# Kernel tuning notes

Measured on AMD Instinct MI355X. Metric: run time of the kernel, lower is better.

## Reference

```python
import jax, jax.numpy as jnp
import numpy as np

B, S, E, H, D = 4, 2048, 1024, 8, 256  # batch, seq, embed_dim, heads, hidden_units


def setup_inputs() -> dict:
    key = jax.random.key(0)
    ks = jax.random.split(key, 9)
    scale = 0.02
    return {
        "inputA": jax.random.normal(ks[0], (B, S, E), dtype=jnp.float32),
        "WQ": jax.random.normal(ks[1], (H, E, D), dtype=jnp.float32) * scale,
        "bQ": jnp.zeros((H, D), dtype=jnp.float32),
        "WK": jax.random.normal(ks[2], (H, E, D), dtype=jnp.float32) * scale,
        "bK": jnp.zeros((H, D), dtype=jnp.float32),
        "WV": jax.random.normal(ks[3], (H, E, D), dtype=jnp.float32) * scale,
        "bV": jnp.zeros((H, D), dtype=jnp.float32),
        "WZ": jax.random.normal(ks[4], (H * D, E), dtype=jnp.float32) * scale,
        "bZ": jnp.zeros((E,), dtype=jnp.float32),
    }


def reference(inputA, WQ, bQ, WK, bK, WV, bV, WZ, bZ):
    # Per-head Linear -> ReLU (dropout=0 -> identity); heads stacked on axis h.
    Q = jax.nn.relu(jnp.einsum('bse,hed->bhsd', inputA, WQ) + bQ[None, :, None, :])
    K = jax.nn.relu(jnp.einsum('bse,hed->bhsd', inputA, WK) + bK[None, :, None, :])
    V = jax.nn.relu(jnp.einsum('bse,hed->bhsd', inputA, WV) + bV[None, :, None, :])
    # scores[b,h,s,t] ; torch bmm output was [B, S, T] per head
    scores = jnp.einsum('bhsd,bhtd->bhst', Q, K) / jnp.sqrt(jnp.float32(E))
    # double softmax: torch dim=1 (query axis s) then dim=2 (key axis t)
    A = jax.nn.softmax(scores, axis=2)
    A = jax.nn.softmax(A, axis=3)
    Z = jnp.einsum('bhst,bhtd->bhsd', A, V)
    # concat heads along feature dim (head order matches torch cat)
    Zall = Z.transpose(0, 2, 1, 3).reshape(B, S, H * D)
    return Zall @ WZ + bZ
```

## Files before the change

### kernel.cpp

```cpp
#include <hip/hip_runtime.h>

typedef __attribute__((ext_vector_type(8))) short short8;
typedef __attribute__((ext_vector_type(4))) float f32x4;

constexpr int B_ = 4, S_ = 2048, E_ = 1024, H_ = 8, D_ = 256;
constexpr int HD_ = H_ * D_;
constexpr int BS_ = B_ * S_;
constexpr int BH_ = B_ * H_;
constexpr float INV_SQRT_E = 0.03125f;

__device__ __forceinline__ unsigned short f2bf(float f) {
    union { float f; unsigned u; } x; x.f = f;
    unsigned r = (x.u + 0x7fffu + ((x.u >> 16) & 1u)) >> 16;
    return (unsigned short)r;
}

__device__ __forceinline__ void gl_lds16(const void* g, void* lds) {
    __builtin_amdgcn_global_load_lds((const __attribute__((address_space(1))) void*)g,
                                     (__attribute__((address_space(3))) void*)lds, 16, 0, 0);
}

__global__ __launch_bounds__(256) void cast_k(const float* __restrict__ src,
                                              unsigned short* __restrict__ dst, int n4) {
    int i = blockIdx.x * 256 + threadIdx.x;
    if (i >= n4) return;
    float4 v = reinterpret_cast<const float4*>(src)[i];
    ushort4 o;
    o.x = f2bf(v.x); o.y = f2bf(v.y); o.z = f2bf(v.z); o.w = f2bf(v.w);
    reinterpret_cast<ushort4*>(dst)[i] = o;
}

__global__ __launch_bounds__(256) void tcast_k(const float* __restrict__ src,
                                               unsigned short* __restrict__ dst, int R, int C) {
    __shared__ float tile[32][33];
    int b = blockIdx.z;
    const float* s = src + (size_t)b * R * C;
    unsigned short* d = dst + (size_t)b * R * C;
    int c0 = blockIdx.x * 32, r0 = blockIdx.y * 32;
    int tx = threadIdx.x, ty = threadIdx.y;
#pragma unroll
    for (int i = 0; i < 4; ++i)
        tile[ty + i * 8][tx] = s[(size_t)(r0 + ty + i * 8) * C + c0 + tx];
    __syncthreads();
#pragma unroll
    for (int i = 0; i < 4; ++i)
        d[(size_t)(c0 + ty + i * 8) * R + r0 + tx] = f2bf(tile[tx][ty + i * 8]);
}

__global__ __launch_bounds__(256) void tbf_k(const unsigned short* __restrict__ src,
                                             unsigned short* __restrict__ dst) {
    __shared__ unsigned short tile[32][33];
    int bh = blockIdx.z;
    int d0 = blockIdx.x * 32, s0 = blockIdx.y * 32;
    int tx = threadIdx.x, ty = threadIdx.y;
#pragma unroll
    for (int i = 0; i < 4; ++i)
        tile[ty + i * 8][tx] = src[((size_t)bh * S_ + s0 + ty + i * 8) * D_ + d0 + tx];
    __syncthreads();
#pragma unroll
    for (int i = 0; i < 4; ++i)
        dst[((size_t)bh * D_ + d0 + ty + i * 8) * S_ + s0 + tx] = tile[tx][ty + i * 8];
}

__global__ __launch_bounds__(256) void gemm_qkv_k(const unsigned short* __restrict__ A,
                                                  const unsigned short* __restrict__ Bt,
                                                  const float* __restrict__ bias,
                                                  unsigned short* __restrict__ out) {
    __shared__ __align__(16) unsigned short As[128 * 32];
    __shared__ __align__(16) unsigned short Bs[128 * 32];
    const int tid = threadIdx.x;
    const int wave = tid >> 6, lane = tid & 63;
    const int quad = lane >> 4, l15 = lane & 15;
    const int wm = wave >> 1, wn = wave & 1;
    const int m0 = blockIdx.y * 128, n0 = blockIdx.x * 128;
    const int c1 = tid, c2 = tid + 256;
    const int r1 = c1 >> 2, kc1 = (c1 & 3) * 8;
    const int r2 = c2 >> 2, kc2 = (c2 & 3) * 8;
    char* aB1 = (char*)As + wave * 1024; char* aB2 = aB1 + 4096;
    char* bB1 = (char*)Bs + wave * 1024; char* bB2 = bB1 + 4096;
    const unsigned short* a1 = A + (size_t)(m0 + r1) * E_ + kc1;
    const unsigned short* a2 = A + (size_t)(m0 + r2) * E_ + kc2;
    const unsigned short* b1 = Bt + (size_t)(n0 + r1) * E_ + kc1;
    const unsigned short* b2 = Bt + (size_t)(n0 + r2) * E_ + kc2;
    f32x4 acc[4][4] = {};
    for (int k0 = 0; k0 < E_; k0 += 32) {
        __syncthreads();
        gl_lds16(a1 + k0, aB1);
        gl_lds16(a2 + k0, aB2);
        gl_lds16(b1 + k0, bB1);
        gl_lds16(b2 + k0, bB2);
        __syncthreads();
        short8 af[4], bf[4];
        const short* Ass = (const short*)As;
        const short* Bss = (const short*)Bs;
#pragma unroll
        for (int f = 0; f < 4; ++f) {
            af[f] = *(const short8*)&Ass[(wm * 64 + f * 16 + l15) * 32 + quad * 8];
            bf[f] = *(const short8*)&Bss[(wn * 64 + f * 16 + l15) * 32 + quad * 8];
        }
#pragma unroll
        for (int fm = 0; fm < 4; ++fm)
#pragma unroll
            for (int fn = 0; fn < 4; ++fn)
                acc[fm][fn] = __builtin_amdgcn_mfma_f32_16x16x32_bf16(af[fm], bf[fn], acc[fm][fn], 0, 0, 0);
    }
#pragma unroll
    for (int fm = 0; fm < 4; ++fm) {
        int mbase = m0 + wm * 64 + fm * 16 + quad * 4;
#pragma unroll
        for (int fn = 0; fn < 4; ++fn) {
            int n = n0 + wn * 64 + fn * 16 + l15;
            int h = n >> 8, d = n & 255;
            float bv = bias[n];
#pragma unroll
            for (int r = 0; r < 4; ++r) {
                int m = mbase + r;
                int b = m >> 11, s = m & 2047;
                float v = fmaxf(acc[fm][fn][r] + bv, 0.0f);
                out[((size_t)(b * H_ + h) * S_ + s) * D_ + d] = f2bf(v);
            }
        }
    }
}

__global__ __launch_bounds__(256) void gemm_out_k(const unsigned short* __restrict__ A,
                                                  const unsigned short* __restrict__ Bt,
                                                  const float* __restrict__ bias,
                                                  float* __restrict__ out) {
    __shared__ __align__(16) unsigned short As[128 * 32];
    __shared__ __align__(16) unsigned short Bs[128 * 32];
    const int tid = threadIdx.x;
    const int wave = tid >> 6, lane = tid & 63;
    const int quad = lane >> 4, l15 = lane & 15;
    const int wm = wave >> 1, wn = wave & 1;
    const int m0 = blockIdx.y * 128, n0 = blockIdx.x * 128;
    const int c1 = tid, c2 = tid + 256;
    const int r1 = c1 >> 2, kc1 = (c1 & 3) * 8;
    const int r2 = c2 >> 2, kc2 = (c2 & 3) * 8;
    char* aB1 = (char*)As + wave * 1024; char* aB2 = aB1 + 4096;
    char* bB1 = (char*)Bs + wave * 1024; char* bB2 = bB1 + 4096;
    const unsigned short* a1 = A + (size_t)(m0 + r1) * HD_ + kc1;
    const unsigned short* a2 = A + (size_t)(m0 + r2) * HD_ + kc2;
    const unsigned short* b1 = Bt + (size_t)(n0 + r1) * HD_ + kc1;
    const unsigned short* b2 = Bt + (size_t)(n0 + r2) * HD_ + kc2;
    f32x4 acc[4][4] = {};
    for (int k0 = 0; k0 < HD_; k0 += 32) {
        __syncthreads();
        gl_lds16(a1 + k0, aB1);
        gl_lds16(a2 + k0, aB2);
        gl_lds16(b1 + k0, bB1);
        gl_lds16(b2 + k0, bB2);
        __syncthreads();
        short8 af[4], bf[4];
        const short* Ass = (const short*)As;
        const short* Bss = (const short*)Bs;
#pragma unroll
        for (int f = 0; f < 4; ++f) {
            af[f] = *(const short8*)&Ass[(wm * 64 + f * 16 + l15) * 32 + quad * 8];
            bf[f] = *(const short8*)&Bss[(wn * 64 + f * 16 + l15) * 32 + quad * 8];
        }
#pragma unroll
        for (int fm = 0; fm < 4; ++fm)
#pragma unroll
            for (int fn = 0; fn < 4; ++fn)
                acc[fm][fn] = __builtin_amdgcn_mfma_f32_16x16x32_bf16(af[fm], bf[fn], acc[fm][fn], 0, 0, 0);
    }
#pragma unroll
    for (int fm = 0; fm < 4; ++fm) {
        int mbase = m0 + wm * 64 + fm * 16 + quad * 4;
#pragma unroll
        for (int fn = 0; fn < 4; ++fn) {
            int n = n0 + wn * 64 + fn * 16 + l15;
            float bv = bias[n];
#pragma unroll
            for (int r = 0; r < 4; ++r)
                out[(size_t)(mbase + r) * E_ + n] = acc[fm][fn][r] + bv;
        }
    }
}

__global__ __launch_bounds__(512, 2) void colsum_k(const unsigned short* __restrict__ Q,
                                                   const unsigned short* __restrict__ K,
                                                   float* __restrict__ invLcol) {
    __shared__ float part[8][64];
    const int tid = threadIdx.x;
    const int wave = tid >> 6, lane = tid & 63;
    const int quad = lane >> 4, l15 = lane & 15;
    const int tg = wave >> 2, sg = wave & 3;
    const int p = blockIdx.x;
    const int bh = (p & 7) + 8 * ((p >> 3) >> 4);
    const int t0 = ((p >> 3) & 15) * 128;
    const unsigned short* Qh = Q + (size_t)bh * S_ * D_;
    const unsigned short* Kh = K + (size_t)bh * S_ * D_;
    short8 kf[32];
#pragma unroll
    for (int kc = 0; kc < 8; ++kc)
#pragma unroll
        for (int fm = 0; fm < 4; ++fm)
            kf[kc * 4 + fm] = *(const short8*)&Kh[(size_t)(t0 + tg * 64 + fm * 16 + l15) * D_ + kc * 32 + quad * 8];
    float rl[4][4] = {};
    const unsigned short* Qw = Qh + (size_t)(sg * 16 + l15) * D_ + quad * 8;
    short8 qf[8];
#pragma unroll
    for (int kc = 0; kc < 8; ++kc) qf[kc] = *(const short8*)&Qw[kc * 32];
    for (int s0 = 0; s0 < S_; s0 += 64) {
        f32x4 acc[4] = {};
#pragma unroll
        for (int kc = 0; kc < 8; ++kc)
#pragma unroll
            for (int fm = 0; fm < 4; ++fm)
                acc[fm] = __builtin_amdgcn_mfma_f32_16x16x32_bf16(kf[kc * 4 + fm], qf[kc], acc[fm], 0, 0, 0);
        int sn = (s0 + 64) & (S_ - 1);
#pragma unroll
        for (int kc = 0; kc < 8; ++kc)
            qf[kc] = *(const short8*)&Qw[(size_t)sn * D_ + kc * 32];
#pragma unroll
        for (int fm = 0; fm < 4; ++fm)
#pragma unroll
            for (int r = 0; r < 4; ++r)
                rl[fm][r] += __expf(acc[fm][r] * INV_SQRT_E);
    }
#pragma unroll
    for (int fm = 0; fm < 4; ++fm)
#pragma unroll
        for (int r = 0; r < 4; ++r) {
            float v = rl[fm][r];
            v += __shfl_xor(v, 1); v += __shfl_xor(v, 2);
            v += __shfl_xor(v, 4); v += __shfl_xor(v, 8);
            if (l15 == 0) part[wave][fm * 16 + quad * 4 + r] = v;
        }
    __syncthreads();
    if (tid < 128) {
        int tg2 = tid >> 6, i = tid & 63;
        float s = part[tg2 * 4 + 0][i] + part[tg2 * 4 + 1][i] +
                  part[tg2 * 4 + 2][i] + part[tg2 * 4 + 3][i];
        invLcol[(size_t)bh * S_ + t0 + tid] = 1.0f / s;
    }
}

__global__ __launch_bounds__(512, 2) void flash10_k(const unsigned short* __restrict__ Q,
                                                    const unsigned short* __restrict__ K,
                                                    const unsigned short* __restrict__ Vt,
                                                    const float* __restrict__ invLcol,
                                                    unsigned short* __restrict__ Zall) {
    __shared__ __align__(16) unsigned short Qs[128 * 136];
    __shared__ __align__(16) unsigned short Ps[2 * 2 * 128 * 40];
    __shared__ float rsum[128];
    const int tid = threadIdx.x;
    const int wave = tid >> 6, lane = tid & 63;
    const int quad = lane >> 4, l15 = lane & 15;
    const int rg = wave >> 2, tc = wave & 3;
    const int dc = wave & 3;
    const int p = blockIdx.x;
    const int bh = (p & 7) + 8 * ((p >> 3) >> 4);
    const int s0 = ((p >> 3) & 15) * 128;
    const int bb = bh >> 3, hh = bh & 7;
    const unsigned short* Qh = Q + (size_t)bh * S_ * D_;
    const unsigned short* Kh = K + (size_t)bh * S_ * D_;
    const unsigned short* Vh = Vt + (size_t)bh * D_ * S_;
    const float* Lc = invLcol + (size_t)bh * S_;

    {
        int row = tid >> 2, cb = (tid & 3) * 128;
        const char* src = (const char*)(Qh + (size_t)(s0 + row) * D_) + cb;
        char* dst = (char*)Qs + row * 272 + cb;
#pragma unroll
        for (int i = 0; i < 8; ++i)
            *(short8*)(dst + i * 16) = *(const short8*)(src + i * 16);
    }
    if (tid < 128) rsum[tid] = 0.f;
    f32x4 zacc[4][4] = {};
    float rsacc[4][4] = {};

    const char* KtBase = (const char*)(Kh + (size_t)(tc * 16 + l15) * D_ + quad * 8);
    const char* VwBase = (const char*)(Vh + (size_t)(dc * 64 + l15) * S_ + quad * 8);
    short8 kb[8], vb[8];
#pragma unroll
    for (int kc = 0; kc < 8; ++kc)
        kb[kc] = *(const short8*)(KtBase + kc * 64);
#pragma unroll
    for (int kk = 0; kk < 2; ++kk)
#pragma unroll
        for (int fn = 0; fn < 4; ++fn)
            vb[kk * 4 + fn] = *(const short8*)(VwBase + ((size_t)(fn * 16) * S_ + kk * 32) * 2);
    float Li = Lc[tc * 16 + l15];
    __syncthreads();

    for (int t0 = 0; t0 < S_; t0 += 64) {
        const int buf = (t0 >> 6) & 1;
        const int tn = (t0 + 64) & (S_ - 1);
        f32x4 acc[4] = {};
#pragma unroll
        for (int kc = 0; kc < 8; ++kc) {
            short8 qa[4];
#pragma unroll
            for (int fm = 0; fm < 4; ++fm)
                qa[fm] = *(const short8*)((const char*)Qs + (rg * 64 + fm * 16 + l15) * 272 + kc * 64 + quad * 16);
#pragma unroll
            for (int fm = 0; fm < 4; ++fm)
                acc[fm] = __builtin_amdgcn_mfma_f32_16x16x32_bf16(qa[fm], kb[kc], acc[fm], 0, 0, 0);
        }
#pragma unroll
        for (int kc = 0; kc < 8; ++kc)
            kb[kc] = *(const short8*)(KtBase + (size_t)tn * (D_ * 2) + kc * 64);
        float Li_n = Lc[tn + tc * 16 + l15];
        unsigned short* Pw = Ps + buf * 10240 + (tc >> 1) * 5120 + (tc & 1) * 16 + l15;
#pragma unroll
        for (int fm = 0; fm < 4; ++fm)
#pragma unroll
            for (int r = 0; r < 4; ++r) {
                float e = __expf(__expf(acc[fm][r] * INV_SQRT_E) * Li);
                rsacc[fm][r] += e;
                int row = rg * 64 + fm * 16 + quad * 4 + r;
                Pw[row * 40] = f2bf(e);
            }
        __syncthreads();
#pragma unroll
        for (int kk = 0; kk < 2; ++kk) {
            short8 pa[4];
#pragma unroll
            for (int fm = 0; fm < 4; ++fm)
                pa[fm] = *(const short8*)&Ps[buf * 10240 + kk * 5120 + (rg * 64 + fm * 16 + l15) * 40 + quad * 8];
#pragma unroll
            for (int fm = 0; fm < 4; ++fm)
#pragma unroll
                for (int fn = 0; fn < 4; ++fn)
                    zacc[fm][fn] = __builtin_amdgcn_mfma_f32_16x16x32_bf16(pa[fm], vb[kk * 4 + fn], zacc[fm][fn], 0, 0, 0);
        }
#pragma unroll
        for (int kk = 0; kk < 2; ++kk)
#pragma unroll
            for (int fn = 0; fn < 4; ++fn)
                vb[kk * 4 + fn] = *(const short8*)(VwBase + ((size_t)(fn * 16) * S_ + tn + kk * 32) * 2);
        Li = Li_n;
    }
#pragma unroll
    for (int fm = 0; fm < 4; ++fm)
#pragma unroll
        for (int r = 0; r < 4; ++r) {
            float v = rsacc[fm][r];
            v += __shfl_xor(v, 1); v += __shfl_xor(v, 2);
            v += __shfl_xor(v, 4); v += __shfl_xor(v, 8);
            if (l15 == 0) atomicAdd(&rsum[rg * 64 + fm * 16 + quad * 4 + r], v);
        }
    __syncthreads();
#pragma unroll
    for (int fm = 0; fm < 4; ++fm)
#pragma unroll
        for (int r = 0; r < 4; ++r) {
            int row = rg * 64 + fm * 16 + quad * 4 + r;
            float inv = 1.0f / rsum[row];
#pragma unroll
            for (int fn = 0; fn < 4; ++fn)
                Zall[(size_t)(bb * S_ + s0 + row) * HD_ + hh * D_ + dc * 64 + fn * 16 + l15] =
                    f2bf(zacc[fm][fn][r] * inv);
        }
}

extern "C" void kernel_launch(void* const* d_in, const int* in_sizes, int n_in,
                              void* d_out, int out_size, void* d_ws, size_t ws_size,
                              hipStream_t stream) {
    const float* Ain = (const float*)d_in[0];
    const float* WQ = (const float*)d_in[1];
    const float* bQ = (const float*)d_in[2];
    const float* WK = (const float*)d_in[3];
    const float* bK = (const float*)d_in[4];
    const float* WV = (const float*)d_in[5];
    const float* bV = (const float*)d_in[6];
    const float* WZ = (const float*)d_in[7];
    const float* bZ = (const float*)d_in[8];
    float* out = (float*)d_out;

    char* ws = (char*)d_ws;
    size_t off = 0;
    auto alloc = [&](size_t bytes) {
        char* p = ws + off;
        off += (bytes + 255) & ~(size_t)255;
        return p;
    };
    unsigned short* Abf = (unsigned short*)alloc((size_t)BS_ * E_ * 2);
    unsigned short* Wqt = (unsigned short*)alloc((size_t)H_ * D_ * E_ * 2);
    unsigned short* Wkt = (unsigned short*)alloc((size_t)H_ * D_ * E_ * 2);
    unsigned short* Wvt = (unsigned short*)alloc((size_t)H_ * D_ * E_ * 2);
    unsigned short* Wzt = (unsigned short*)alloc((size_t)E_ * HD_ * 2);
    unsigned short* Qb = (unsigned short*)alloc((size_t)BH_ * S_ * D_ * 2);
    unsigned short* Kb = (unsigned short*)alloc((size_t)BH_ * S_ * D_ * 2);
    unsigned short* Vb = (unsigned short*)alloc((size_t)BH_ * S_ * D_ * 2);
    unsigned short* Vtb = (unsigned short*)alloc((size_t)BH_ * S_ * D_ * 2);
    unsigned short* Zb = (unsigned short*)alloc((size_t)BS_ * HD_ * 2);
    float* Lc = (float*)alloc((size_t)BH_ * S_ * 4);

    dim3 tb(32, 8);
    cast_k<<<(BS_ * E_ / 4 + 255) / 256, 256, 0, stream>>>(Ain, Abf, BS_ * E_ / 4);
    tcast_k<<<dim3(D_ / 32, E_ / 32, H_), tb, 0, stream>>>(WQ, Wqt, E_, D_);
    tcast_k<<<dim3(D_ / 32, E_ / 32, H_), tb, 0, stream>>>(WK, Wkt, E_, D_);
    tcast_k<<<dim3(D_ / 32, E_ / 32, H_), tb, 0, stream>>>(WV, Wvt, E_, D_);
    tcast_k<<<dim3(E_ / 32, HD_ / 32, 1), tb, 0, stream>>>(WZ, Wzt, HD_, E_);

    gemm_qkv_k<<<dim3(HD_ / 128, BS_ / 128), 256, 0, stream>>>(Abf, Wqt, bQ, Qb);
    gemm_qkv_k<<<dim3(HD_ / 128, BS_ / 128), 256, 0, stream>>>(Abf, Wkt, bK, Kb);
    gemm_qkv_k<<<dim3(HD_ / 128, BS_ / 128), 256, 0, stream>>>(Abf, Wvt, bV, Vb);

    tbf_k<<<dim3(D_ / 32, S_ / 32, BH_), tb, 0, stream>>>(Vb, Vtb);

    colsum_k<<<dim3(BH_ * S_ / 128), 512, 0, stream>>>(Qb, Kb, Lc);
    flash10_k<<<dim3(BH_ * S_ / 128), 512, 0, stream>>>(Qb, Kb, Vtb, Lc, Zb);

    gemm_out_k<<<dim3(E_ / 128, BS_ / 128), 256, 0, stream>>>(Zb, Wzt, bZ, out);
}
```

Before: 723.8 us.

## Widen flash attention key tile to 128 with streamed K prefetch

The attention kernel now processes 128 keys per iteration instead of 64, so each wave computes two 16-column score tiles per Q fragment read from LDS. K fragments are refilled inside the QK loop in a rotating register scheme rather than in one batch afterward. The P tile becomes a single 128x128 LDS buffer, and the PV product is split into two halves with V reloads between them. The change halves the Q LDS reads and barriers per key, but drops P double buffering, so an extra barrier is needed each iteration.

```diff
diff --git a/kernel.cpp b/kernel.cpp
--- a/kernel.cpp
+++ b/kernel.cpp
@@ -238,13 +238,13 @@
     }
 }
 
-__global__ __launch_bounds__(512, 2) void flash10_k(const unsigned short* __restrict__ Q,
+__global__ __launch_bounds__(512, 2) void flash11_k(const unsigned short* __restrict__ Q,
                                                     const unsigned short* __restrict__ K,
                                                     const unsigned short* __restrict__ Vt,
                                                     const float* __restrict__ invLcol,
                                                     unsigned short* __restrict__ Zall) {
     __shared__ __align__(16) unsigned short Qs[128 * 136];
-    __shared__ __align__(16) unsigned short Ps[2 * 2 * 128 * 40];
+    __shared__ __align__(16) unsigned short Ps[128 * 132];
     __shared__ float rsum[128];
     const int tid = threadIdx.x;
     const int wave = tid >> 6, lane = tid & 63;
@@ -272,47 +272,56 @@
     f32x4 zacc[4][4] = {};
     float rsacc[4][4] = {};
 
-    const char* KtBase = (const char*)(Kh + (size_t)(tc * 16 + l15) * D_ + quad * 8);
-    const char* VwBase = (const char*)(Vh + (size_t)(dc * 64 + l15) * S_ + quad * 8);
+    const unsigned short* KtW = Kh + (size_t)(tc * 32 + l15) * D_ + quad * 8;
+    const unsigned short* VwBase = Vh + (size_t)(dc * 64 + l15) * S_ + quad * 8;
     short8 kb[8], vb[8];
 #pragma unroll
-    for (int kc = 0; kc < 8; ++kc)
-        kb[kc] = *(const short8*)(KtBase + kc * 64);
+    for (int f = 0; f < 8; ++f)
+        kb[f] = *(const short8*)&KtW[(size_t)((f & 1) * 16) * D_ + (f >> 1) * 32];
 #pragma unroll
     for (int kk = 0; kk < 2; ++kk)
 #pragma unroll
         for (int fn = 0; fn < 4; ++fn)
-            vb[kk * 4 + fn] = *(const short8*)(VwBase + ((size_t)(fn * 16) * S_ + kk * 32) * 2);
-    float Li = Lc[tc * 16 + l15];
+            vb[kk * 4 + fn] = *(const short8*)&VwBase[(size_t)(fn * 16) * S_ + kk * 32];
+    float Li0 = Lc[tc * 32 + l15];
+    float Li1 = Lc[tc * 32 + 16 + l15];
     __syncthreads();
 
-    for (int t0 = 0; t0 < S_; t0 += 64) {
-        const int buf = (t0 >> 6) & 1;
-        const int tn = (t0 + 64) & (S_ - 1);
-        f32x4 acc[4] = {};
+    for (int t0 = 0; t0 < S_; t0 += 128) {
+        const int tn = (t0 + 128) & (S_ - 1);
+        f32x4 acc[4][2] = {};
 #pragma unroll
         for (int kc = 0; kc < 8; ++kc) {
             short8 qa[4];
 #pragma unroll
             for (int fm = 0; fm < 4; ++fm)
                 qa[fm] = *(const short8*)((const char*)Qs + (rg * 64 + fm * 16 + l15) * 272 + kc * 64 + quad * 16);
-#pragma unroll
-            for (int fm = 0; fm < 4; ++fm)
-                acc[fm] = __builtin_amdgcn_mfma_f32_16x16x32_bf16(qa[fm], kb[kc], acc[fm], 0, 0, 0);
-        }
-#pragma unroll
-        for (int kc = 0; kc < 8; ++kc)
-            kb[kc] = *(const short8*)(KtBase + (size_t)tn * (D_ * 2) + kc * 64);
-        float Li_n = Lc[tn + tc * 16 + l15];
-        unsigned short* Pw = Ps + buf * 10240 + (tc >> 1) * 5120 + (tc & 1) * 16 + l15;
+            short8 k0 = kb[(2 * kc) & 7], k1 = kb[(2 * kc + 1) & 7];
+            if (kc < 4) {
+                kb[(2 * kc) & 7]     = *(const short8*)&KtW[(size_t)(t0 + 0)  * D_ + (size_t)(kc + 4) * 32];
+                kb[(2 * kc + 1) & 7] = *(const short8*)&KtW[(size_t)(t0 + 16) * D_ + (size_t)(kc + 4) * 32];
+            } else {
+                kb[(2 * kc) & 7]     = *(const short8*)&KtW[(size_t)(tn + 0)  * D_ + (size_t)(kc - 4) * 32];
+                kb[(2 * kc + 1) & 7] = *(const short8*)&KtW[(size_t)(tn + 16) * D_ + (size_t)(kc - 4) * 32];
+            }
+#pragma unroll
+            for (int fm = 0; fm < 4; ++fm) {
+                acc[fm][0] = __builtin_amdgcn_mfma_f32_16x16x32_bf16(qa[fm], k0, acc[fm][0], 0, 0, 0);
+                acc[fm][1] = __builtin_amdgcn_mfma_f32_16x16x32_bf16(qa[fm], k1, acc[fm][1], 0, 0, 0);
+            }
+        }
+        float Li0n = Lc[tn + tc * 32 + l15];
+        float Li1n = Lc[tn + tc * 32 + 16 + l15];
 #pragma unroll
         for (int fm = 0; fm < 4; ++fm)
 #pragma unroll
             for (int r = 0; r < 4; ++r) {
-                float e = __expf(__expf(acc[fm][r] * INV_SQRT_E) * Li);
-                rsacc[fm][r] += e;
                 int row = rg * 64 + fm * 16 + quad * 4 + r;
-                Pw[row * 40] = f2bf(e);
+                float e0 = __expf(__expf(acc[fm][0][r] * INV_SQRT_E) * Li0);
+                float e1 = __expf(__expf(acc[fm][1][r] * INV_SQRT_E) * Li1);
+                rsacc[fm][r] += e0 + e1;
+                Ps[row * 132 + tc * 32 + l15] = f2bf(e0);
+                Ps[row * 132 + tc * 32 + 16 + l15] = f2bf(e1);
             }
         __syncthreads();
 #pragma unroll
@@ -320,7 +329,7 @@
             short8 pa[4];
 #pragma unroll
             for (int fm = 0; fm < 4; ++fm)
-                pa[fm] = *(const short8*)&Ps[buf * 10240 + kk * 5120 + (rg * 64 + fm * 16 + l15) * 40 + quad * 8];
+                pa[fm] = *(const short8*)&Ps[(rg * 64 + fm * 16 + l15) * 132 + kk * 32 + quad * 8];
 #pragma unroll
             for (int fm = 0; fm < 4; ++fm)
 #pragma unroll
@@ -331,8 +340,26 @@
         for (int kk = 0; kk < 2; ++kk)
 #pragma unroll
             for (int fn = 0; fn < 4; ++fn)
-                vb[kk * 4 + fn] = *(const short8*)(VwBase + ((size_t)(fn * 16) * S_ + tn + kk * 32) * 2);
-        Li = Li_n;
+                vb[kk * 4 + fn] = *(const short8*)&VwBase[(size_t)(fn * 16) * S_ + t0 + (kk + 2) * 32];
+#pragma unroll
+        for (int kk = 0; kk < 2; ++kk) {
+            short8 pa[4];
+#pragma unroll
+            for (int fm = 0; fm < 4; ++fm)
+                pa[fm] = *(const short8*)&Ps[(rg * 64 + fm * 16 + l15) * 132 + (kk + 2) * 32 + quad * 8];
+#pragma unroll
+            for (int fm = 0; fm < 4; ++fm)
+#pragma unroll
+                for (int fn = 0; fn < 4; ++fn)
+                    zacc[fm][fn] = __builtin_amdgcn_mfma_f32_16x16x32_bf16(pa[fm], vb[kk * 4 + fn], zacc[fm][fn], 0, 0, 0);
+        }
+#pragma unroll
+        for (int kk = 0; kk < 2; ++kk)
+#pragma unroll
+            for (int fn = 0; fn < 4; ++fn)
+                vb[kk * 4 + fn] = *(const short8*)&VwBase[(size_t)(fn * 16) * S_ + tn + kk * 32];
+        __syncthreads();
+        Li0 = Li0n; Li1 = Li1n;
     }
 #pragma unroll
     for (int fm = 0; fm < 4; ++fm)
@@ -404,7 +431,7 @@
     tbf_k<<<dim3(D_ / 32, S_ / 32, BH_), tb, 0, stream>>>(Vb, Vtb);
 
     colsum_k<<<dim3(BH_ * S_ / 128), 512, 0, stream>>>(Qb, Kb, Lc);
-    flash10_k<<<dim3(BH_ * S_ / 128), 512, 0, stream>>>(Qb, Kb, Vtb, Lc, Zb);
+    flash11_k<<<dim3(BH_ * S_ / 128), 512, 0, stream>>>(Qb, Kb, Vtb, Lc, Zb);
 
     gemm_out_k<<<dim3(E_ / 128, BS_ / 128), 256, 0, stream>>>(Zb, Wzt, bZ, out);
 }
```

Result: no change. 723.7 us (-0.0%).
